# Kernel optimization log

Hardware: AMD Instinct MI355X
Metric: run time of the kernel (lower is better)

Reference implementation:

```python
import jax, jax.numpy as jnp
import numpy as np

B, S, D, UNITS = 64, 2048, 512, 256

def setup_inputs() -> dict:
    key = jax.random.key(0)
    ks = jax.random.split(key, 8)
    sd = 1.0 / np.sqrt(D)
    query = jax.random.normal(ks[0], (B, D), dtype=jnp.float32)
    values = jax.random.normal(ks[1], (B, S, D), dtype=jnp.float32)
    W1 = jax.random.normal(ks[2], (D, UNITS), dtype=jnp.float32) * sd
    b1 = jnp.zeros((UNITS,), dtype=jnp.float32)
    W2 = jax.random.normal(ks[3], (D, UNITS), dtype=jnp.float32) * sd
    b2 = jnp.zeros((UNITS,), dtype=jnp.float32)
    V = jax.random.normal(ks[4], (UNITS, 1), dtype=jnp.float32) * (1.0 / np.sqrt(UNITS))
    bV = jnp.zeros((1,), dtype=jnp.float32)
    return {"query": query, "values": values, "W1": W1, "b1": b1,
            "W2": W2, "b2": b2, "V": V, "bV": bV}

def reference(query, values, W1, b1, W2, b2, V, bV):
    # proj_v: [B, S, U]; proj_q: [B, 1, U]
    proj_v = jnp.einsum('bsd,du->bsu', values, W1) + b1
    proj_q = (query @ W2 + b2)[:, None, :]
    # score: [B, S, 1]
    score = jnp.tanh(proj_v + proj_q) @ V + bV
    attn = jax.nn.softmax(score, axis=1)           # softmax over sequence axis
    context = jnp.sum(attn * values, axis=1)        # [B, D]
    return context
```

## Files before the change

### kernel.cpp

```cpp
#include <hip/hip_runtime.h>
#include <hip/hip_bf16.h>

typedef unsigned short u16;
typedef unsigned int u32;
typedef __attribute__((ext_vector_type(8))) short short8;
typedef __attribute__((ext_vector_type(4))) float f32x4;

#define NB 64
#define NS 2048
#define ND 512
#define NU 256
#define ASTR 520

__device__ __forceinline__ u16 f2b(float f) {
    u32 x = __float_as_uint(f);
    u32 r = (x + 0x7FFFu + ((x >> 16) & 1u)) >> 16;
    return (u16)r;
}
__device__ __forceinline__ u32 pk2(float lo, float hi) {
    __hip_bfloat162 h = __float22bfloat162_rn(float2{lo, hi});
    return *(u32*)&h;
}
__device__ __forceinline__ float fast_tanh(float x) {
    float e = __expf(2.0f * x);
    return 1.0f - 2.0f / (e + 1.0f);
}

__global__ __launch_bounds__(256) void cbias_kernel(
    const float* __restrict__ q, const float* __restrict__ W2,
    const float* __restrict__ b1, const float* __restrict__ b2,
    float* __restrict__ cb)
{
    int b = blockIdx.x, u = threadIdx.x;
    __shared__ float qs[ND];
    qs[u]       = q[b * ND + u];
    qs[u + 256] = q[b * ND + u + 256];
    __syncthreads();
    float acc = 0.f;
#pragma unroll 8
    for (int d = 0; d < ND; d++)
        acc += qs[d] * W2[d * NU + u];
    cb[b * NU + u] = acc + b1[u] + b2[u];
}

__global__ __launch_bounds__(256) void transpose_kernel(
    const float* __restrict__ W1, u16* __restrict__ W1Tc)
{
    __shared__ float tile[64][65];
    int k0 = blockIdx.x * 64;
    int u0 = blockIdx.y * 64;
    for (int i = threadIdx.x; i < 4096; i += 256) {
        int r = i >> 6, c = i & 63;
        tile[r][c] = W1[(k0 + r) * NU + u0 + c];
    }
    __syncthreads();
    for (int i = threadIdx.x; i < 4096; i += 256) {
        int r = i >> 6, c = i & 63;
        W1Tc[blockIdx.x * (NU * 64) + (u0 + r) * 64 + c] = f2b(tile[c][r]);
    }
}

__global__ __launch_bounds__(256, 2) void fused_kernel(
    const float* __restrict__ values,
    const u16* __restrict__ W1Tc,
    const float* __restrict__ cb,
    const float* __restrict__ V,
    float* __restrict__ ctxp,
    float2* __restrict__ meta)
{
    const int tid  = threadIdx.x;
    const int lane = tid & 63;
    const int wn   = tid >> 6;
    const int m16  = lane & 15;
    const int quad = lane >> 4;

    const int mblk = blockIdx.x;
    const int b    = mblk >> 5;
    const size_t base_row = (size_t)mblk * 64;

    __shared__ u16 Afull[64][ASTR];
    __shared__ float cbs[NU];
    __shared__ float Vs[NU];
    __shared__ float rowsum[64];
    __shared__ float wsm[64];
    __shared__ float mred[2];

    cbs[tid] = cb[b * NU + tid];
    Vs[tid]  = V[tid];
    if (tid < 64) rowsum[tid] = 0.f;

    f32x4 acc[4][4] = {};

    const float* asrc = values + (base_row + (tid >> 2)) * ND + (tid & 3) * 16;
    const int arow = tid >> 2, acol = (tid & 3) * 16;

    float4 v0 = ((const float4*)asrc)[0];
    float4 v1 = ((const float4*)asrc)[1];
    float4 v2 = ((const float4*)asrc)[2];
    float4 v3 = ((const float4*)asrc)[3];

    for (int kc = 0; kc < 8; kc++) {
        {
            uint4 q0, q1;
            q0.x = pk2(v0.x, v0.y); q0.y = pk2(v0.z, v0.w);
            q0.z = pk2(v1.x, v1.y); q0.w = pk2(v1.z, v1.w);
            q1.x = pk2(v2.x, v2.y); q1.y = pk2(v2.z, v2.w);
            q1.z = pk2(v3.x, v3.y); q1.w = pk2(v3.z, v3.w);
            *(uint4*)&Afull[arow][kc * 64 + acol]     = q0;
            *(uint4*)&Afull[arow][kc * 64 + acol + 8] = q1;
        }
        __syncthreads();
        if (kc < 7) {
            const float* nsrc = asrc + (kc + 1) * 64;
            v0 = ((const float4*)nsrc)[0];
            v1 = ((const float4*)nsrc)[1];
            v2 = ((const float4*)nsrc)[2];
            v3 = ((const float4*)nsrc)[3];
        }
        short8 bfr[2][4];
#pragma unroll
        for (int kh = 0; kh < 2; kh++)
#pragma unroll
            for (int cbk = 0; cbk < 4; cbk++)
                bfr[kh][cbk] = *(const short8*)(W1Tc + (size_t)kc * (NU * 64)
                                + (wn * 64 + cbk * 16 + m16) * 64 + kh * 32 + quad * 8);
#pragma unroll
        for (int kh = 0; kh < 2; kh++) {
            short8 afr[4];
#pragma unroll
            for (int rb = 0; rb < 4; rb++)
                afr[rb] = *(const short8*)&Afull[rb * 16 + m16][kc * 64 + kh * 32 + quad * 8];
#pragma unroll
            for (int rb = 0; rb < 4; rb++)
#pragma unroll
                for (int cbk = 0; cbk < 4; cbk++)
                    acc[rb][cbk] = __builtin_amdgcn_mfma_f32_16x16x32_bf16(
                        afr[rb], bfr[kh][cbk], acc[rb][cbk], 0, 0, 0);
        }
        __syncthreads();
    }

    float cbv[4], vv[4];
#pragma unroll
    for (int cbk = 0; cbk < 4; cbk++) {
        int c = wn * 64 + cbk * 16 + m16;
        cbv[cbk] = cbs[c];
        vv[cbk]  = Vs[c];
    }
#pragma unroll
    for (int rb = 0; rb < 4; rb++) {
#pragma unroll
        for (int i = 0; i < 4; i++) {
            float s = 0.f;
#pragma unroll
            for (int cbk = 0; cbk < 4; cbk++)
                s += fast_tanh(acc[rb][cbk][i] + cbv[cbk]) * vv[cbk];
            s += __shfl_xor(s, 1, 64);
            s += __shfl_xor(s, 2, 64);
            s += __shfl_xor(s, 4, 64);
            s += __shfl_xor(s, 8, 64);
            if (m16 == 0)
                atomicAdd(&rowsum[rb * 16 + quad * 4 + i], s);
        }
    }
    __syncthreads();

    if (tid < 64) {
        float s = rowsum[tid];
        float m = s;
        m = fmaxf(m, __shfl_xor(m, 1, 64));
        m = fmaxf(m, __shfl_xor(m, 2, 64));
        m = fmaxf(m, __shfl_xor(m, 4, 64));
        m = fmaxf(m, __shfl_xor(m, 8, 64));
        m = fmaxf(m, __shfl_xor(m, 16, 64));
        m = fmaxf(m, __shfl_xor(m, 32, 64));
        float w = __expf(s - m);
        wsm[tid] = w;
        float l = w;
        l += __shfl_xor(l, 1, 64);
        l += __shfl_xor(l, 2, 64);
        l += __shfl_xor(l, 4, 64);
        l += __shfl_xor(l, 8, 64);
        l += __shfl_xor(l, 16, 64);
        l += __shfl_xor(l, 32, 64);
        if (tid == 0) { mred[0] = m; mred[1] = l; }
    }
    __syncthreads();

    {
        const u32* adw = (const u32*)&Afull[0][0];
        float a0 = 0.f, a1 = 0.f;
#pragma unroll 8
        for (int r = 0; r < 64; r++) {
            u32 pk = adw[r * (ASTR / 2) + tid];
            float lo = __uint_as_float(pk << 16);
            float hi = __uint_as_float(pk & 0xFFFF0000u);
            float wt = wsm[r];
            a0 += wt * lo;
            a1 += wt * hi;
        }
        float* dst = ctxp + (size_t)mblk * ND + tid * 2;
        dst[0] = a0;
        dst[1] = a1;
    }
    if (tid == 0) meta[mblk] = float2{mred[0], mred[1]};
}

__global__ __launch_bounds__(256) void combine_kernel(
    const float* __restrict__ ctxp, const float2* __restrict__ meta,
    float* __restrict__ out)
{
    int b = blockIdx.x, tid = threadIdx.x;
    __shared__ float wc[32];
    __shared__ float Ls;
    if (tid == 0) {
        float M = -1e30f;
        for (int c = 0; c < 32; c++) M = fmaxf(M, meta[b * 32 + c].x);
        float L = 0.f;
        for (int c = 0; c < 32; c++) {
            float w = __expf(meta[b * 32 + c].x - M);
            wc[c] = w;
            L += w * meta[b * 32 + c].y;
        }
        Ls = L;
    }
    __syncthreads();
    float inv = 1.0f / Ls;
    float s0 = 0.f, s1 = 0.f;
#pragma unroll 4
    for (int c = 0; c < 32; c++) {
        const float* p = ctxp + ((size_t)b * 32 + c) * ND;
        float w = wc[c];
        s0 += w * p[tid];
        s1 += w * p[tid + 256];
    }
    out[b * ND + tid]       = s0 * inv;
    out[b * ND + tid + 256] = s1 * inv;
}

extern "C" void kernel_launch(void* const* d_in, const int* in_sizes, int n_in,
                              void* d_out, int out_size, void* d_ws, size_t ws_size,
                              hipStream_t stream)
{
    const float* q      = (const float*)d_in[0];
    const float* values = (const float*)d_in[1];
    const float* W1     = (const float*)d_in[2];
    const float* b1     = (const float*)d_in[3];
    const float* W2     = (const float*)d_in[4];
    const float* b2     = (const float*)d_in[5];
    const float* V      = (const float*)d_in[6];

    char* ws = (char*)d_ws;
    float*  cb    = (float*) (ws);
    u16*    W1Tc  = (u16*)   (ws + 65536);
    float*  ctxp  = (float*) (ws + 327680);
    float2* meta  = (float2*)(ws + 327680 + 4194304);

    hipLaunchKernelGGL(cbias_kernel, dim3(64), dim3(256), 0, stream, q, W2, b1, b2, cb);
    hipLaunchKernelGGL(transpose_kernel, dim3(8, 4), dim3(256), 0, stream, W1, W1Tc);
    hipLaunchKernelGGL(fused_kernel, dim3(2048), dim3(256), 0, stream,
                       values, W1Tc, cb, V, ctxp, meta);
    hipLaunchKernelGGL(combine_kernel, dim3(64), dim3(256), 0, stream,
                       ctxp, meta, (float*)d_out);
}
```

Baseline: 461.1 us.

## Halve rows per block to 32 and raise occupancy to four blocks per CU

The fused kernel now handles 32 sequence rows per block instead of 64, which doubles the grid to 4096 blocks, halves the LDS tile and accumulator registers, and raises launch bounds to four blocks per CU. The trailing __syncthreads in the k-loop is removed because each k-chunk writes a distinct LDS column range. The combine kernel now reduces 64 partials per batch with a wavefront shuffle instead of a serial loop on one thread. The cost is that every block re-reads the full W1 bf16 matrix, doubling that traffic, and the partial-context buffer in the workspace doubles in size.

```diff
diff --git a/kernel.cpp b/kernel.cpp
--- a/kernel.cpp
+++ b/kernel.cpp
@@ -10,6 +10,8 @@
 #define NS 2048
 #define ND 512
 #define NU 256
+#define CH 32
+#define CPB (NS / CH)
 #define ASTR 520
 
 __device__ __forceinline__ u16 f2b(float f) {
@@ -60,7 +62,7 @@
     }
 }
 
-__global__ __launch_bounds__(256, 2) void fused_kernel(
+__global__ __launch_bounds__(256, 4) void fused_kernel(
     const float* __restrict__ values,
     const u16* __restrict__ W1Tc,
     const float* __restrict__ cb,
@@ -75,47 +77,40 @@
     const int quad = lane >> 4;
 
     const int mblk = blockIdx.x;
-    const int b    = mblk >> 5;
-    const size_t base_row = (size_t)mblk * 64;
-
-    __shared__ u16 Afull[64][ASTR];
+    const int b    = mblk >> 6;
+    const size_t base_row = (size_t)mblk * CH;
+
+    __shared__ u16 Afull[CH][ASTR];
     __shared__ float cbs[NU];
     __shared__ float Vs[NU];
-    __shared__ float rowsum[64];
-    __shared__ float wsm[64];
+    __shared__ float rowsum[CH];
+    __shared__ float wsm[CH];
     __shared__ float mred[2];
 
     cbs[tid] = cb[b * NU + tid];
     Vs[tid]  = V[tid];
-    if (tid < 64) rowsum[tid] = 0.f;
-
-    f32x4 acc[4][4] = {};
-
-    const float* asrc = values + (base_row + (tid >> 2)) * ND + (tid & 3) * 16;
-    const int arow = tid >> 2, acol = (tid & 3) * 16;
+    if (tid < CH) rowsum[tid] = 0.f;
+
+    f32x4 acc[2][4] = {};
+
+    const int arow = tid >> 3, acol = (tid & 7) * 8;
+    const float* asrc = values + (base_row + arow) * ND + acol;
 
     float4 v0 = ((const float4*)asrc)[0];
     float4 v1 = ((const float4*)asrc)[1];
-    float4 v2 = ((const float4*)asrc)[2];
-    float4 v3 = ((const float4*)asrc)[3];
 
     for (int kc = 0; kc < 8; kc++) {
         {
-            uint4 q0, q1;
+            uint4 q0;
             q0.x = pk2(v0.x, v0.y); q0.y = pk2(v0.z, v0.w);
             q0.z = pk2(v1.x, v1.y); q0.w = pk2(v1.z, v1.w);
-            q1.x = pk2(v2.x, v2.y); q1.y = pk2(v2.z, v2.w);
-            q1.z = pk2(v3.x, v3.y); q1.w = pk2(v3.z, v3.w);
-            *(uint4*)&Afull[arow][kc * 64 + acol]     = q0;
-            *(uint4*)&Afull[arow][kc * 64 + acol + 8] = q1;
+            *(uint4*)&Afull[arow][kc * 64 + acol] = q0;
         }
         __syncthreads();
         if (kc < 7) {
             const float* nsrc = asrc + (kc + 1) * 64;
             v0 = ((const float4*)nsrc)[0];
             v1 = ((const float4*)nsrc)[1];
-            v2 = ((const float4*)nsrc)[2];
-            v3 = ((const float4*)nsrc)[3];
         }
         short8 bfr[2][4];
 #pragma unroll
@@ -126,18 +121,17 @@
                                 + (wn * 64 + cbk * 16 + m16) * 64 + kh * 32 + quad * 8);
 #pragma unroll
         for (int kh = 0; kh < 2; kh++) {
-            short8 afr[4];
-#pragma unroll
-            for (int rb = 0; rb < 4; rb++)
+            short8 afr[2];
+#pragma unroll
+            for (int rb = 0; rb < 2; rb++)
                 afr[rb] = *(const short8*)&Afull[rb * 16 + m16][kc * 64 + kh * 32 + quad * 8];
 #pragma unroll
-            for (int rb = 0; rb < 4; rb++)
+            for (int rb = 0; rb < 2; rb++)
 #pragma unroll
                 for (int cbk = 0; cbk < 4; cbk++)
                     acc[rb][cbk] = __builtin_amdgcn_mfma_f32_16x16x32_bf16(
                         afr[rb], bfr[kh][cbk], acc[rb][cbk], 0, 0, 0);
         }
-        __syncthreads();
     }
 
     float cbv[4], vv[4];
@@ -148,7 +142,7 @@
         vv[cbk]  = Vs[c];
     }
 #pragma unroll
-    for (int rb = 0; rb < 4; rb++) {
+    for (int rb = 0; rb < 2; rb++) {
 #pragma unroll
         for (int i = 0; i < 4; i++) {
             float s = 0.f;
@@ -165,7 +159,7 @@
     }
     __syncthreads();
 
-    if (tid < 64) {
+    if (tid < CH) {
         float s = rowsum[tid];
         float m = s;
         m = fmaxf(m, __shfl_xor(m, 1, 64));
@@ -173,7 +167,6 @@
         m = fmaxf(m, __shfl_xor(m, 4, 64));
         m = fmaxf(m, __shfl_xor(m, 8, 64));
         m = fmaxf(m, __shfl_xor(m, 16, 64));
-        m = fmaxf(m, __shfl_xor(m, 32, 64));
         float w = __expf(s - m);
         wsm[tid] = w;
         float l = w;
@@ -182,7 +175,6 @@
         l += __shfl_xor(l, 4, 64);
         l += __shfl_xor(l, 8, 64);
         l += __shfl_xor(l, 16, 64);
-        l += __shfl_xor(l, 32, 64);
         if (tid == 0) { mred[0] = m; mred[1] = l; }
     }
     __syncthreads();
@@ -191,7 +183,7 @@
         const u32* adw = (const u32*)&Afull[0][0];
         float a0 = 0.f, a1 = 0.f;
 #pragma unroll 8
-        for (int r = 0; r < 64; r++) {
+        for (int r = 0; r < CH; r++) {
             u32 pk = adw[r * (ASTR / 2) + tid];
             float lo = __uint_as_float(pk << 16);
             float hi = __uint_as_float(pk & 0xFFFF0000u);
@@ -199,9 +191,8 @@
             a0 += wt * lo;
             a1 += wt * hi;
         }
-        float* dst = ctxp + (size_t)mblk * ND + tid * 2;
-        dst[0] = a0;
-        dst[1] = a1;
+        float2* dst = (float2*)(ctxp + (size_t)mblk * ND + tid * 2);
+        *dst = float2{a0, a1};
     }
     if (tid == 0) meta[mblk] = float2{mred[0], mred[1]};
 }
@@ -211,25 +202,34 @@
     float* __restrict__ out)
 {
     int b = blockIdx.x, tid = threadIdx.x;
-    __shared__ float wc[32];
+    __shared__ float wc[CPB];
     __shared__ float Ls;
-    if (tid == 0) {
-        float M = -1e30f;
-        for (int c = 0; c < 32; c++) M = fmaxf(M, meta[b * 32 + c].x);
-        float L = 0.f;
-        for (int c = 0; c < 32; c++) {
-            float w = __expf(meta[b * 32 + c].x - M);
-            wc[c] = w;
-            L += w * meta[b * 32 + c].y;
-        }
-        Ls = L;
+    if (tid < CPB) {
+        float2 mt = meta[b * CPB + tid];
+        float m = mt.x;
+        m = fmaxf(m, __shfl_xor(m, 1, 64));
+        m = fmaxf(m, __shfl_xor(m, 2, 64));
+        m = fmaxf(m, __shfl_xor(m, 4, 64));
+        m = fmaxf(m, __shfl_xor(m, 8, 64));
+        m = fmaxf(m, __shfl_xor(m, 16, 64));
+        m = fmaxf(m, __shfl_xor(m, 32, 64));
+        float w = __expf(mt.x - m);
+        wc[tid] = w;
+        float l = w * mt.y;
+        l += __shfl_xor(l, 1, 64);
+        l += __shfl_xor(l, 2, 64);
+        l += __shfl_xor(l, 4, 64);
+        l += __shfl_xor(l, 8, 64);
+        l += __shfl_xor(l, 16, 64);
+        l += __shfl_xor(l, 32, 64);
+        if (tid == 0) Ls = l;
     }
     __syncthreads();
     float inv = 1.0f / Ls;
     float s0 = 0.f, s1 = 0.f;
 #pragma unroll 4
-    for (int c = 0; c < 32; c++) {
-        const float* p = ctxp + ((size_t)b * 32 + c) * ND;
+    for (int c = 0; c < CPB; c++) {
+        const float* p = ctxp + ((size_t)b * CPB + c) * ND;
         float w = wc[c];
         s0 += w * p[tid];
         s1 += w * p[tid + 256];
@@ -254,11 +254,11 @@
     float*  cb    = (float*) (ws);
     u16*    W1Tc  = (u16*)   (ws + 65536);
     float*  ctxp  = (float*) (ws + 327680);
-    float2* meta  = (float2*)(ws + 327680 + 4194304);
+    float2* meta  = (float2*)(ws + 327680 + 8388608);
 
     hipLaunchKernelGGL(cbias_kernel, dim3(64), dim3(256), 0, stream, q, W2, b1, b2, cb);
     hipLaunchKernelGGL(transpose_kernel, dim3(8, 4), dim3(256), 0, stream, W1, W1Tc);
-    hipLaunchKernelGGL(fused_kernel, dim3(2048), dim3(256), 0, stream,
+    hipLaunchKernelGGL(fused_kernel, dim3(NB * CPB), dim3(256), 0, stream,
                        values, W1Tc, cb, V, ctxp, meta);
     hipLaunchKernelGGL(combine_kernel, dim3(64), dim3(256), 0, stream,
                        ctxp, meta, (float*)d_out);
```

After: 498.2 us. +8.0%, slower.
